# Kernel tuning notes

Hardware: AMD Instinct MI355X
Metric: run time of the kernel (lower is better)

Reference implementation:

```python
import jax, jax.numpy as jnp
import numpy as np

COMMITMENT_COST = 0.25


def setup_inputs() -> dict:
    key = jax.random.key(0)
    k1, k2 = jax.random.split(key)
    z = jax.random.normal(k1, (4096, 512), dtype=jnp.float32)
    # stacked codebooks: [num_codebooks, codebook_size, latent_dim]
    codebooks = jax.random.normal(k2, (8, 16384, 512), dtype=jnp.float32)
    return {"z": z, "codebooks": codebooks}


def reference(z, codebooks):
    """Residual VQ forward. Returns (quantized [B,D], loss scalar, indices [B,K])."""
    z_sg = jax.lax.stop_gradient(z)

    def step(carry, cb):
        residual, quantized, loss = carry
        # squared L2 distances: [B, C]
        d = (jnp.sum(residual * residual, axis=1, keepdims=True)
             + jnp.sum(cb * cb, axis=1)
             - 2.0 * (residual @ cb.T))
        idx = jnp.argmin(d, axis=1)              # [B]
        q_i = cb[idx]                            # gather: [B, D]
        commitment = COMMITMENT_COST * jnp.mean((jax.lax.stop_gradient(q_i) - z) ** 2)
        codebook_l = jnp.mean((q_i - z_sg) ** 2)
        loss = loss + commitment + codebook_l
        return (residual - q_i, quantized + q_i, loss), idx

    init = (z, jnp.zeros_like(z), jnp.float32(0.0))
    (_, quantized, loss), idxs = jax.lax.scan(step, init, codebooks)
    return quantized, loss, idxs.T  # indices: [B, num_codebooks]
```

## Files before the change

kernel.cpp:

```cpp
#include <hip/hip_runtime.h>

typedef _Float16 half8 __attribute__((ext_vector_type(8)));
typedef _Float16 half4v __attribute__((ext_vector_type(4)));
typedef float f32x4 __attribute__((ext_vector_type(4)));

#define MFMA_F16 __builtin_amdgcn_mfma_f32_16x16x32_f16

static constexpr int BATCH  = 4096;
static constexpr int DIM    = 512;
static constexpr int CODES  = 16384;
static constexpr int NCB    = 8;
static constexpr int NCHUNK = 8;
static constexpr int CHUNK  = CODES / NCHUNK;
static constexpr int NT     = CHUNK / 16;
static constexpr int HTILES = NT / 2;
static constexpr int NGROUP = HTILES / 2;
static constexpr int BM     = 128;
static constexpr int NPC    = NCHUNK * 2 * 2;
static constexpr int TILE_H = 8192;
static constexpr int TILE_B = 16384;
static constexpr float LO_SCALE = 2048.0f;
static constexpr float LO_INV   = 1.0f / 2048.0f;
static constexpr float DELTA    = 0.25f;

__device__ __forceinline__ int swz(int code, int kk) {
  return code * DIM + (kk ^ (((code ^ (kk >> 6)) & 7) << 3));
}

__global__ __launch_bounds__(256) void k_init(const float* __restrict__ z,
                                              float* __restrict__ resid,
                                              _Float16* __restrict__ rhi,
                                              _Float16* __restrict__ rlo) {
  int i = blockIdx.x * 256 + threadIdx.x;
  float4 v = ((const float4*)z)[i];
  ((float4*)resid)[i] = v;
  half4v h, l;
  const float* vf = (const float*)&v;
#pragma unroll
  for (int j = 0; j < 4; ++j) {
    float x = vf[j];
    _Float16 hi = (_Float16)x;
    h[j] = hi;
    l[j] = (_Float16)((x - (float)hi) * LO_SCALE);
  }
  *(half4v*)&rhi[(size_t)i * 4] = h;
  *(half4v*)&rlo[(size_t)i * 4] = l;
}

__global__ __launch_bounds__(256) void k_cnorm(const float* __restrict__ cb,
                                               float* __restrict__ cnorm) {
  int wave = threadIdx.x >> 6, lane = threadIdx.x & 63;
  int code = blockIdx.x * 4 + wave;
  const float4* src = (const float4*)(cb + (size_t)code * DIM);
  double s = 0.0;
#pragma unroll
  for (int j = 0; j < 2; ++j) {
    float4 v = src[lane * 2 + j];
    s += (double)v.x * v.x + (double)v.y * v.y + (double)v.z * v.z + (double)v.w * v.w;
  }
#pragma unroll
  for (int off = 32; off; off >>= 1) s += __shfl_down(s, off);
  if (lane == 0) cnorm[code] = (float)s;
}

__global__ __launch_bounds__(256) void k_cvtn(const float* __restrict__ cb,
                                              _Float16* __restrict__ dst,
                                              float* __restrict__ cnorm_k) {
  const int wave  = threadIdx.x >> 6;
  const int lane  = threadIdx.x & 63;
  const int chunk = blockIdx.x & 7;
  const int cidx  = (blockIdx.x >> 3) * 4 + wave;
  const int ntile = cidx >> 4;
  const int code  = cidx & 15;
  const int code_g = chunk * CHUNK + cidx;

  const float* src = cb + (size_t)code_g * DIM + lane * 8;
  float4 v0 = *(const float4*)src;
  float4 v1 = *(const float4*)(src + 4);
  half8 h;
  const float* f0 = (const float*)&v0;
  const float* f1 = (const float*)&v1;
  double s = 0.0;
#pragma unroll
  for (int e = 0; e < 4; ++e) {
    float x = f0[e];
    h[e] = (_Float16)x;
    s += (double)x * x;
    x = f1[e];
    h[e + 4] = (_Float16)x;
    s += (double)x * x;
  }
  const int pos = (lane >> 2) * 512 + (lane & 3) * 128 + code * 8;
  *(half8*)(dst + (size_t)(chunk * NT + ntile) * TILE_H + pos) = h;

#pragma unroll
  for (int off = 32; off; off >>= 1) s += __shfl_down(s, off);
  if (lane == 0) cnorm_k[code_g] = (float)s;
}

#define LEXLT(av, ai, bv, bi) ((av) < (bv) || ((av) == (bv) && (ai) < (bi)))

__global__ __launch_bounds__(256, 2) void k_argmin_pc(
    const _Float16* __restrict__ rhi,
    const _Float16* __restrict__ cvt,
    const float* __restrict__ cnorm,
    float* __restrict__ partmin, int* __restrict__ partidx) {
  __shared__ float Xs[2][4][6][64][4];

  const int tid   = threadIdx.x;
  const int lane  = tid & 63;
  const int kq    = tid >> 6;
  const int chunk = blockIdx.x & 7;
  const int idx   = blockIdx.x >> 3;
  const int mtile = idx >> 1;
  const int half  = idx & 1;
  const int nt0   = half * HTILES;
  const int cbase = chunk * CHUNK;
  const char* ctile = (const char*)(cvt + (size_t)chunk * NT * TILE_H);

  const int kb = (lane >> 4) * 8;
  half8 ah[8][4];
#pragma unroll
  for (int band = 0; band < 8; ++band) {
    const size_t rbase =
        (size_t)(mtile * BM + band * 16 + (lane & 15)) * DIM + kq * 128;
#pragma unroll
    for (int t = 0; t < 4; ++t)
      ah[band][t] = *(const half8*)(rhi + rbase + t * 32 + kb);
  }

  const int qbase = kq * 4096 + lane * 16;
  const int rcode = lane & 15;

  float tv0[2][4], tv1[2][4];
  int   ti0[2][4], ti1[2][4];
#pragma unroll
  for (int j = 0; j < 2; ++j)
#pragma unroll
    for (int r = 0; r < 4; ++r) {
      tv0[j][r] = tv1[j][r] = 3.4e38f;
      ti0[j][r] = ti1[j][r] = 0x7fffffff;
    }

  half8 s0h[2], s1h[2];

#define LOAD_HT(SH, NTI, H)                                                  \
  {                                                                          \
    const char* bp_ = ctile + (size_t)(NTI) * TILE_B + qbase + (H) * 2048;   \
    SH[0] = *(const half8*)(bp_);                                            \
    SH[1] = *(const half8*)(bp_ + 1024);                                     \
  }

#define MFMA_HT(SH, TB)                                                      \
  {                                                                          \
    __builtin_amdgcn_s_setprio(1);                                           \
    _Pragma("unroll")                                                        \
    for (int j_ = 0; j_ < 2; ++j_) {                                         \
      _Pragma("unroll")                                                      \
      for (int b_ = 0; b_ < 8; ++b_)                                         \
        acch[b_] = MFMA_F16(ah[b_][(TB) + j_], SH[j_], acch[b_], 0, 0, 0);   \
    }                                                                        \
    __builtin_amdgcn_s_setprio(0);                                           \
  }

#define TOP2_INS(d, cg, J, R)                                                \
  {                                                                          \
    bool b0_ = (d) < tv0[J][R];                                              \
    bool b1_ = (d) < tv1[J][R];                                              \
    tv1[J][R] = b0_ ? tv0[J][R] : (b1_ ? (d) : tv1[J][R]);                   \
    ti1[J][R] = b0_ ? ti0[J][R] : (b1_ ? (cg) : ti1[J][R]);                  \
    tv0[J][R] = b0_ ? (d) : tv0[J][R];                                       \
    ti0[J][R] = b0_ ? (cg) : ti0[J][R];                                      \
  }

  LOAD_HT(s0h, nt0, 0);
  float cn_a = cnorm[cbase + nt0 * 16 + rcode];
  float cn_b = cnorm[cbase + (nt0 + 1) * 16 + rcode];

  for (int g = 0; g < NGROUP; ++g) {
    const int ta = nt0 + 2 * g;
    const int tb = ta + 1;
    const bool more = (g + 1 < NGROUP);
    float cn_na = more ? cnorm[cbase + (ta + 2) * 16 + rcode] : 0.f;
    float cn_nb = more ? cnorm[cbase + (ta + 3) * 16 + rcode] : 0.f;

    f32x4 acch[8];
    f32x4 dha0, dha1, dhb0, dhb1;

#pragma unroll
    for (int b = 0; b < 8; ++b) acch[b] = (f32x4){0.f, 0.f, 0.f, 0.f};
    LOAD_HT(s1h, ta, 1);
    MFMA_HT(s0h, 0);
    LOAD_HT(s0h, tb, 0);
    MFMA_HT(s1h, 2);
#pragma unroll
    for (int b = 0; b < 8; ++b) {
      if ((b >> 1) == kq) {
        if ((b & 1) == 0) dha0 = acch[b]; else dha1 = acch[b];
      } else {
        const int slot = b - (((b >> 1) > kq) ? 2 : 0);
        *(f32x4*)&Xs[0][kq][slot][lane][0] = acch[b];
      }
    }

#pragma unroll
    for (int b = 0; b < 8; ++b) acch[b] = (f32x4){0.f, 0.f, 0.f, 0.f};
    LOAD_HT(s1h, tb, 1);
    MFMA_HT(s0h, 0);
    const int pn = more ? ta + 2 : tb;
    LOAD_HT(s0h, pn, 0);
    MFMA_HT(s1h, 2);
#pragma unroll
    for (int b = 0; b < 8; ++b) {
      if ((b >> 1) == kq) {
        if ((b & 1) == 0) dhb0 = acch[b]; else dhb1 = acch[b];
      } else {
        const int slot = b - (((b >> 1) > kq) ? 2 : 0);
        *(f32x4*)&Xs[1][kq][slot][lane][0] = acch[b];
      }
    }

    asm volatile("s_waitcnt lgkmcnt(0)" ::: "memory");
    __builtin_amdgcn_s_barrier();
    __builtin_amdgcn_sched_barrier(0);

    f32x4 dta[2] = {dha0, dha1};
    f32x4 dtb[2] = {dhb0, dhb1};
#pragma unroll
    for (int j = 0; j < 2; ++j) {
      const int ob = 2 * kq + j;
      for (int kq2 = 0; kq2 < 4; ++kq2) {
        if (kq2 == kq) continue;
        const int slot = ob - ((kq > kq2) ? 2 : 0);
        dta[j] += *(const f32x4*)&Xs[0][kq2][slot][lane][0];
        dtb[j] += *(const f32x4*)&Xs[1][kq2][slot][lane][0];
      }
    }
    __builtin_amdgcn_sched_barrier(0);
    __builtin_amdgcn_s_barrier();
    __builtin_amdgcn_sched_barrier(0);

    const int cga = cbase + ta * 16 + rcode;
    const int cgb = cga + 16;
#pragma unroll
    for (int j = 0; j < 2; ++j) {
#pragma unroll
      for (int r = 0; r < 4; ++r) {
        float d = cn_a - 2.0f * dta[j][r];
        TOP2_INS(d, cga, j, r);
      }
#pragma unroll
      for (int r = 0; r < 4; ++r) {
        float d = cn_b - 2.0f * dtb[j][r];
        TOP2_INS(d, cgb, j, r);
      }
    }
    cn_a = cn_na;
    cn_b = cn_nb;
  }
#undef LOAD_HT
#undef MFMA_HT
#undef TOP2_INS

#pragma unroll
  for (int s = 1; s < 16; s <<= 1) {
#pragma unroll
    for (int j = 0; j < 2; ++j) {
#pragma unroll
      for (int r = 0; r < 4; ++r) {
        float b0v = __shfl_xor(tv0[j][r], s), b1v = __shfl_xor(tv1[j][r], s);
        int   b0i = __shfl_xor(ti0[j][r], s), b1i = __shfl_xor(ti1[j][r], s);
        bool p0 = LEXLT(tv0[j][r], ti0[j][r], b0v, b0i);
        float r0v = p0 ? tv0[j][r] : b0v;  int r0i = p0 ? ti0[j][r] : b0i;
        float xv  = p0 ? b0v : tv0[j][r];  int xi  = p0 ? b0i : ti0[j][r];
        bool p1 = LEXLT(tv1[j][r], ti1[j][r], b1v, b1i);
        float yv = p1 ? tv1[j][r] : b1v;   int yi = p1 ? ti1[j][r] : b1i;
        bool p2 = LEXLT(xv, xi, yv, yi);
        float r1v = p2 ? xv : yv;          int r1i = p2 ? xi : yi;
        tv0[j][r] = r0v; ti0[j][r] = r0i;
        tv1[j][r] = r1v; ti1[j][r] = r1i;
      }
    }
  }
  if ((lane & 15) == 0) {
    const int pslot = chunk * 2 + half;
#pragma unroll
    for (int j = 0; j < 2; ++j) {
      const int rowbase = mtile * BM + (2 * kq + j) * 16 + (lane >> 4) * 4;
#pragma unroll
      for (int r = 0; r < 4; ++r) {
        const size_t base = (size_t)(rowbase + r) * NPC + pslot * 2;
        partmin[base + 0] = tv0[j][r]; partidx[base + 0] = ti0[j][r];
        partmin[base + 1] = tv1[j][r]; partidx[base + 1] = ti1[j][r];
      }
    }
  }
}

__device__ __forceinline__ void load8(const float* __restrict__ cb, int cbase, int nt,
                                      int s_code, int s_kseg, float4 v[8]) {
  const float4* src = (const float4*)(cb + (size_t)(cbase + nt * 16 + s_code) * DIM + s_kseg);
#pragma unroll
  for (int j = 0; j < 8; ++j) v[j] = src[j];
}

__device__ __forceinline__ void cvt_store(_Float16* __restrict__ BHbuf,
                                          _Float16* __restrict__ BLbuf,
                                          int code, int kseg, const float4 sv[8]) {
  const float* f = (const float*)sv;
#pragma unroll
  for (int j = 0; j < 4; ++j) {
    half8 h, l;
#pragma unroll
    for (int e = 0; e < 8; ++e) {
      float x = f[j * 8 + e];
      _Float16 hi = (_Float16)x;
      h[e] = hi;
      l[e] = (_Float16)((x - (float)hi) * LO_SCALE);
    }
    int hw = swz(code, kseg + j * 8);
    *(half8*)(BHbuf + hw) = h;
    *(half8*)(BLbuf + hw) = l;
  }
}

__global__ __launch_bounds__(256, 2) void k_argmin_fb(
    const _Float16* __restrict__ rhi, const _Float16* __restrict__ rlo,
    const float* __restrict__ cb, const float* __restrict__ cnorm,
    float* __restrict__ partmin, int* __restrict__ partidx) {
  __shared__ _Float16 BH[2][16 * DIM];
  __shared__ _Float16 BL[2][16 * DIM];
  __shared__ float CN[CHUNK];

  const int tid   = threadIdx.x;
  const int lane  = tid & 63;
  const int wave  = tid >> 6;
  const int mtile = blockIdx.x >> 3;
  const int chunk = blockIdx.x & 7;
  const int cbase = chunk * CHUNK;

  {
    const float4* s = (const float4*)(cnorm + cbase);
    float4* d = (float4*)CN;
    for (int i = tid; i < CHUNK / 4; i += 256) d[i] = s[i];
  }

  const int arow = mtile * 64 + wave * 16 + (lane & 15);
  const int kb = (lane >> 4) * 8;
  half8 ah[16], al[16];
#pragma unroll
  for (int t = 0; t < 16; ++t) {
    ah[t] = *(const half8*)(rhi + (size_t)arow * DIM + t * 32 + kb);
    al[t] = *(const half8*)(rlo + (size_t)arow * DIM + t * 32 + kb);
  }

  const int s_code = tid >> 4;
  const int s_kseg = (tid & 15) * 32;

  float rmin[4] = {3.4e38f, 3.4e38f, 3.4e38f, 3.4e38f};
  int   ridx[4] = {0, 0, 0, 0};

  {
    float4 v0[8];
    load8(cb, cbase, 0, s_code, s_kseg, v0);
    cvt_store(&BH[0][0], &BL[0][0], s_code, s_kseg, v0);
  }

  const int rcode = lane & 15;
  for (int nt = 0; nt < NT; ++nt) {
    __syncthreads();
    const int cur = nt & 1;
    const bool more = (nt + 1 < NT);
    float4 nv[8];
    if (more) load8(cb, cbase, nt + 1, s_code, s_kseg, nv);

    f32x4 acch  = {0.f, 0.f, 0.f, 0.f};
    f32x4 accl0 = {0.f, 0.f, 0.f, 0.f};
    f32x4 accl1 = {0.f, 0.f, 0.f, 0.f};
    const _Float16* bh = &BH[cur][0];
    const _Float16* bl = &BL[cur][0];
#pragma unroll
    for (int t = 0; t < 16; ++t) {
      const int hw = swz(rcode, t * 32 + kb);
      half8 fbh = *(const half8*)(bh + hw);
      half8 fbl = *(const half8*)(bl + hw);
      acch  = MFMA_F16(ah[t], fbh, acch, 0, 0, 0);
      accl0 = MFMA_F16(ah[t], fbl, accl0, 0, 0, 0);
      accl1 = MFMA_F16(al[t], fbh, accl1, 0, 0, 0);
    }
    float cn = CN[nt * 16 + rcode];
    int codeg = cbase + nt * 16 + rcode;
#pragma unroll
    for (int r = 0; r < 4; ++r) {
      float d = cn - 2.0f * (acch[r] + (accl0[r] + accl1[r]) * LO_INV);
      if (d < rmin[r]) { rmin[r] = d; ridx[r] = codeg; }
    }
    if (more) cvt_store(&BH[cur ^ 1][0], &BL[cur ^ 1][0], s_code, s_kseg, nv);
  }

#pragma unroll
  for (int s = 1; s < 16; s <<= 1) {
#pragma unroll
    for (int r = 0; r < 4; ++r) {
      float ov = __shfl_xor(rmin[r], s);
      int   oi = __shfl_xor(ridx[r], s);
      if (ov < rmin[r] || (ov == rmin[r] && oi < ridx[r])) { rmin[r] = ov; ridx[r] = oi; }
    }
  }
  if ((lane & 15) == 0) {
    int rowbase = mtile * 64 + wave * 16 + (lane >> 4) * 4;
#pragma unroll
    for (int r = 0; r < 4; ++r) {
#pragma unroll
      for (int t = 0; t < 4; ++t) {
        partmin[(size_t)(rowbase + r) * NPC + chunk * 4 + t] = rmin[r];
        partidx[(size_t)(rowbase + r) * NPC + chunk * 4 + t] = ridx[r];
      }
    }
  }
}

__global__ __launch_bounds__(256) void k_update(
    const float* __restrict__ cb, const float* __restrict__ z,
    const float* __restrict__ partmin, const int* __restrict__ partidx,
    float* __restrict__ resid, _Float16* __restrict__ rhi, _Float16* __restrict__ rlo,
    float* __restrict__ quant, float* __restrict__ out_idx,
    float* __restrict__ losspart, int step) {
  __shared__ int   s_idx[16];
  __shared__ int   s_cand[16][32];
  __shared__ int   s_cnt[16];
  __shared__ float s_red[4];
  const int tid = threadIdx.x;
  const int row0 = blockIdx.x * 16;

  if (tid < 16) {
    const int row = row0 + tid;
    float m = 3.4e38f;
    for (int c = 0; c < NPC; ++c) {
      float v = partmin[(size_t)row * NPC + c];
      if (v < m) m = v;
    }
    int cnt = 0;
    for (int c = 0; c < NPC; ++c) {
      float v = partmin[(size_t)row * NPC + c];
      if (v < m + DELTA) s_cand[tid][cnt++] = partidx[(size_t)row * NPC + c];
    }
    s_cnt[tid] = cnt;
  }
  __syncthreads();

  {
    const int wv = tid >> 6, ln = tid & 63;
    for (int rr = wv; rr < 16; rr += 4) {
      const int row = row0 + rr;
      const float* rrow = resid + (size_t)row * DIM + ln * 8;
      double bestd = 1.0e300;
      int    besti = 0x7fffffff;
      const int cnt = s_cnt[rr];
      for (int c = 0; c < cnt; ++c) {
        const int ci = s_cand[rr][c];
        const float* crow = cb + (size_t)ci * DIM + ln * 8;
        double s = 0.0;
#pragma unroll
        for (int e = 0; e < 8; ++e) {
          double df = (double)rrow[e] - (double)crow[e];
          s += df * df;
        }
#pragma unroll
        for (int off = 32; off; off >>= 1) s += __shfl_down(s, off);
        s = __shfl(s, 0);
        if (s < bestd || (s == bestd && ci < besti)) { bestd = s; besti = ci; }
      }
      if (ln == 0) {
        s_idx[rr] = besti;
        out_idx[(size_t)row * NCB + step] = (float)besti;
      }
    }
  }
  __syncthreads();

  float lsum = 0.f;
  const int sub = tid >> 7;
  const int e   = tid & 127;
  for (int rp = 0; rp < 16; rp += 2) {
    const int rl = rp + sub;
    const int row = row0 + rl;
    const int idx = s_idx[rl];
    float4 q  = ((const float4*)cb)[(size_t)idx * 128 + e];
    float4 zv = ((const float4*)z)[(size_t)row * 128 + e];
    float4 rv = ((const float4*)resid)[(size_t)row * 128 + e];
    float4 nr, qa;
    const float* qf = (const float*)&q;
    const float* zf = (const float*)&zv;
    const float* rf = (const float*)&rv;
    float* nf = (float*)&nr;
    float* af = (float*)&qa;
    if (step == 0) {
#pragma unroll
      for (int j = 0; j < 4; ++j) af[j] = qf[j];
    } else {
      float4 old = ((const float4*)quant)[(size_t)row * 128 + e];
      const float* of = (const float*)&old;
#pragma unroll
      for (int j = 0; j < 4; ++j) af[j] = of[j] + qf[j];
    }
    ((float4*)quant)[(size_t)row * 128 + e] = qa;
    half4v h, l;
#pragma unroll
    for (int j = 0; j < 4; ++j) {
      float nrj = rf[j] - qf[j];
      nf[j] = nrj;
      _Float16 hi = (_Float16)nrj;
      h[j] = hi;
      l[j] = (_Float16)((nrj - (float)hi) * LO_SCALE);
      float dq = qf[j] - zf[j];
      lsum += dq * dq;
    }
    ((float4*)resid)[(size_t)row * 128 + e] = nr;
    *(half4v*)&rhi[(size_t)row * DIM + e * 4] = h;
    *(half4v*)&rlo[(size_t)row * DIM + e * 4] = l;
  }
#pragma unroll
  for (int off = 32; off; off >>= 1) lsum += __shfl_down(lsum, off);
  if ((tid & 63) == 0) s_red[tid >> 6] = lsum;
  __syncthreads();
  if (tid == 0) losspart[blockIdx.x] = s_red[0] + s_red[1] + s_red[2] + s_red[3];
}

__global__ __launch_bounds__(256) void k_loss(const float* __restrict__ losspart,
                                              float* __restrict__ out_loss) {
  __shared__ double red[4];
  const int tid = threadIdx.x;
  double s = 0.0;
  for (int i = tid; i < NCB * 256; i += 256) s += (double)losspart[i];
#pragma unroll
  for (int off = 32; off; off >>= 1) s += __shfl_down(s, off);
  if ((tid & 63) == 0) red[tid >> 6] = s;
  __syncthreads();
  if (tid == 0)
    out_loss[0] = (float)((red[0] + red[1] + red[2] + red[3]) *
                          (1.25 / (double)((size_t)BATCH * DIM)));
}

extern "C" void kernel_launch(void* const* d_in, const int* in_sizes, int n_in,
                              void* d_out, int out_size, void* d_ws, size_t ws_size,
                              hipStream_t stream) {
  const float* z  = (const float*)d_in[0];
  const float* cb = (const float*)d_in[1];
  float* out = (float*)d_out;
  float* quant    = out;
  float* out_loss = out + (size_t)BATCH * DIM;
  float* out_idx  = out + (size_t)BATCH * DIM + 1;

  char* ws = (char*)d_ws;
  float*    resid    = (float*)ws;
  _Float16* rhi      = (_Float16*)(ws + ((size_t)8  << 20));
  _Float16* rlo      = (_Float16*)(ws + ((size_t)12 << 20));
  float*    cnorm    = (float*)(ws + ((size_t)16 << 20));
  float*    partmin  = (float*)(ws + ((size_t)17 << 20));
  int*      partidx  = (int*)  (ws + ((size_t)18 << 20));
  float*    losspart = (float*)(ws + ((size_t)19 << 20));
  _Float16* cvtbuf   = (_Float16*)(ws + ((size_t)20 << 20));

  const size_t REQ = ((size_t)20 << 20) + ((size_t)16 << 20);
  const bool pre = (ws_size >= REQ);

  k_init<<<dim3((BATCH * DIM / 4) / 256), dim3(256), 0, stream>>>(z, resid, rhi, rlo);
  if (!pre)
    k_cnorm<<<dim3(NCB * CODES / 4), dim3(256), 0, stream>>>(cb, cnorm);

  for (int k = 0; k < NCB; ++k) {
    const float* cbk = cb + (size_t)k * CODES * DIM;
    if (pre) {
      k_cvtn<<<dim3(CODES * 64 / 256), dim3(256), 0, stream>>>(
          cbk, cvtbuf, cnorm + (size_t)k * CODES);
      k_argmin_pc<<<dim3((BATCH / BM) * NCHUNK * 2), dim3(256), 0, stream>>>(
          rhi, cvtbuf, cnorm + (size_t)k * CODES, partmin, partidx);
    } else {
      k_argmin_fb<<<dim3((BATCH / 64) * NCHUNK), dim3(256), 0, stream>>>(
          rhi, rlo, cbk, cnorm + (size_t)k * CODES, partmin, partidx);
    }
    k_update<<<dim3(BATCH / 16), dim3(256), 0, stream>>>(
        cbk, z, partmin, partidx, resid, rhi, rlo,
        quant, out_idx, losspart + k * 256, k);
  }
  k_loss<<<dim3(1), dim3(256), 0, stream>>>(losspart, out_loss);
}
```

Before: 993.2 us.

## Split argmin waves into 2 row-groups by 2 K-halves to cut LDS reduction

The argmin kernel's work split across the four waves changes from four K-quarters covering all 8 row bands to two K-halves times two row-groups of 4 bands each. Each wave now computes 4 band accumulators over 256 of K instead of 8 over 128. The cross-wave partial-sum exchange through shared memory falls from 6 stores and 6 loads per tile pair to 2 of each with one partner wave. In exchange each wave loads twice as many codebook fragments per tile, and the total MFMA count stays the same.

Result: slower. 2.566 ms (+158.3%).

```diff
diff --git a/kernel.cpp b/kernel.cpp
--- a/kernel.cpp
+++ b/kernel.cpp
@@ -105,11 +105,14 @@
     const _Float16* __restrict__ cvt,
     const float* __restrict__ cnorm,
     float* __restrict__ partmin, int* __restrict__ partidx) {
-  __shared__ float Xs[2][4][6][64][4];
+  __shared__ float Xs[2][4][2][64][4];
 
   const int tid   = threadIdx.x;
   const int lane  = tid & 63;
-  const int kq    = tid >> 6;
+  const int wave  = tid >> 6;
+  const int wp    = wave >> 1;
+  const int kh    = wave & 1;
+  const int partner = wp * 2 + (kh ^ 1);
   const int chunk = blockIdx.x & 7;
   const int idx   = blockIdx.x >> 3;
   const int mtile = idx >> 1;
@@ -119,18 +122,20 @@
   const char* ctile = (const char*)(cvt + (size_t)chunk * NT * TILE_H);
 
   const int kb = (lane >> 4) * 8;
-  half8 ah[8][4];
-#pragma unroll
-  for (int band = 0; band < 8; ++band) {
+  half8 ah[4][8];
+#pragma unroll
+  for (int lb = 0; lb < 4; ++lb) {
     const size_t rbase =
-        (size_t)(mtile * BM + band * 16 + (lane & 15)) * DIM + kq * 128;
-#pragma unroll
-    for (int t = 0; t < 4; ++t)
-      ah[band][t] = *(const half8*)(rhi + rbase + t * 32 + kb);
-  }
-
-  const int qbase = kq * 4096 + lane * 16;
+        (size_t)(mtile * BM + (4 * wp + lb) * 16 + (lane & 15)) * DIM + kh * 256;
+#pragma unroll
+    for (int t = 0; t < 8; ++t)
+      ah[lb][t] = *(const half8*)(rhi + rbase + t * 32 + kb);
+  }
+
+  const int qbase = kh * 8192 + lane * 16;
   const int rcode = lane & 15;
+
+  const int ownbase = kh * 2;
 
   float tv0[2][4], tv1[2][4];
   int   ti0[2][4], ti1[2][4];
@@ -142,22 +147,24 @@
       ti0[j][r] = ti1[j][r] = 0x7fffffff;
     }
 
-  half8 s0h[2], s1h[2];
+  half8 s0h[4], s1h[4];
 
 #define LOAD_HT(SH, NTI, H)                                                  \
   {                                                                          \
-    const char* bp_ = ctile + (size_t)(NTI) * TILE_B + qbase + (H) * 2048;   \
+    const char* bp_ = ctile + (size_t)(NTI) * TILE_B + qbase + (H) * 4096;   \
     SH[0] = *(const half8*)(bp_);                                            \
     SH[1] = *(const half8*)(bp_ + 1024);                                     \
+    SH[2] = *(const half8*)(bp_ + 2048);                                     \
+    SH[3] = *(const half8*)(bp_ + 3072);                                     \
   }
 
 #define MFMA_HT(SH, TB)                                                      \
   {                                                                          \
     __builtin_amdgcn_s_setprio(1);                                           \
     _Pragma("unroll")                                                        \
-    for (int j_ = 0; j_ < 2; ++j_) {                                         \
+    for (int j_ = 0; j_ < 4; ++j_) {                                         \
       _Pragma("unroll")                                                      \
-      for (int b_ = 0; b_ < 8; ++b_)                                         \
+      for (int b_ = 0; b_ < 4; ++b_)                                         \
         acch[b_] = MFMA_F16(ah[b_][(TB) + j_], SH[j_], acch[b_], 0, 0, 0);   \
     }                                                                        \
     __builtin_amdgcn_s_setprio(0);                                           \
@@ -184,58 +191,48 @@
     float cn_na = more ? cnorm[cbase + (ta + 2) * 16 + rcode] : 0.f;
     float cn_nb = more ? cnorm[cbase + (ta + 3) * 16 + rcode] : 0.f;
 
-    f32x4 acch[8];
-    f32x4 dha0, dha1, dhb0, dhb1;
-
-#pragma unroll
-    for (int b = 0; b < 8; ++b) acch[b] = (f32x4){0.f, 0.f, 0.f, 0.f};
+    f32x4 acch[4];
+    f32x4 owna0, owna1, ownb0, ownb1;
+
+#pragma unroll
+    for (int b = 0; b < 4; ++b) acch[b] = (f32x4){0.f, 0.f, 0.f, 0.f};
     LOAD_HT(s1h, ta, 1);
     MFMA_HT(s0h, 0);
     LOAD_HT(s0h, tb, 0);
-    MFMA_HT(s1h, 2);
-#pragma unroll
-    for (int b = 0; b < 8; ++b) {
-      if ((b >> 1) == kq) {
-        if ((b & 1) == 0) dha0 = acch[b]; else dha1 = acch[b];
-      } else {
-        const int slot = b - (((b >> 1) > kq) ? 2 : 0);
-        *(f32x4*)&Xs[0][kq][slot][lane][0] = acch[b];
-      }
-    }
-
-#pragma unroll
-    for (int b = 0; b < 8; ++b) acch[b] = (f32x4){0.f, 0.f, 0.f, 0.f};
+    MFMA_HT(s1h, 4);
+    owna0 = acch[ownbase];
+    owna1 = acch[ownbase + 1];
+    {
+      const int fb = 2 - ownbase;
+      *(f32x4*)&Xs[0][wave][0][lane][0] = acch[fb];
+      *(f32x4*)&Xs[0][wave][1][lane][0] = acch[fb + 1];
+    }
+
+#pragma unroll
+    for (int b = 0; b < 4; ++b) acch[b] = (f32x4){0.f, 0.f, 0.f, 0.f};
     LOAD_HT(s1h, tb, 1);
     MFMA_HT(s0h, 0);
     const int pn = more ? ta + 2 : tb;
     LOAD_HT(s0h, pn, 0);
-    MFMA_HT(s1h, 2);
-#pragma unroll
-    for (int b = 0; b < 8; ++b) {
-      if ((b >> 1) == kq) {
-        if ((b & 1) == 0) dhb0 = acch[b]; else dhb1 = acch[b];
-      } else {
-        const int slot = b - (((b >> 1) > kq) ? 2 : 0);
-        *(f32x4*)&Xs[1][kq][slot][lane][0] = acch[b];
-      }
+    MFMA_HT(s1h, 4);
+    ownb0 = acch[ownbase];
+    ownb1 = acch[ownbase + 1];
+    {
+      const int fb = 2 - ownbase;
+      *(f32x4*)&Xs[1][wave][0][lane][0] = acch[fb];
+      *(f32x4*)&Xs[1][wave][1][lane][0] = acch[fb + 1];
     }
 
     asm volatile("s_waitcnt lgkmcnt(0)" ::: "memory");
     __builtin_amdgcn_s_barrier();
     __builtin_amdgcn_sched_barrier(0);
 
-    f32x4 dta[2] = {dha0, dha1};
-    f32x4 dtb[2] = {dhb0, dhb1};
-#pragma unroll
-    for (int j = 0; j < 2; ++j) {
-      const int ob = 2 * kq + j;
-      for (int kq2 = 0; kq2 < 4; ++kq2) {
-        if (kq2 == kq) continue;
-        const int slot = ob - ((kq > kq2) ? 2 : 0);
-        dta[j] += *(const f32x4*)&Xs[0][kq2][slot][lane][0];
-        dtb[j] += *(const f32x4*)&Xs[1][kq2][slot][lane][0];
-      }
-    }
+    f32x4 dta[2], dtb[2];
+    dta[0] = owna0 + *(const f32x4*)&Xs[0][partner][0][lane][0];
+    dta[1] = owna1 + *(const f32x4*)&Xs[0][partner][1][lane][0];
+    dtb[0] = ownb0 + *(const f32x4*)&Xs[1][partner][0][lane][0];
+    dtb[1] = ownb1 + *(const f32x4*)&Xs[1][partner][1][lane][0];
+
     __builtin_amdgcn_sched_barrier(0);
     __builtin_amdgcn_s_barrier();
     __builtin_amdgcn_sched_barrier(0);
@@ -286,7 +283,8 @@
     const int pslot = chunk * 2 + half;
 #pragma unroll
     for (int j = 0; j < 2; ++j) {
-      const int rowbase = mtile * BM + (2 * kq + j) * 16 + (lane >> 4) * 4;
+      const int gband = 4 * wp + ownbase + j;
+      const int rowbase = mtile * BM + gband * 16 + (lane >> 4) * 4;
 #pragma unroll
       for (int r = 0; r < 4; ++r) {
         const size_t base = (size_t)(rowbase + r) * NPC + pslot * 2;
```

## Convert all codebooks upfront and split argmin into quarter-chunk blocks

Applied to the files above, without the earlier changes.

Moves the fp16 conversion of all eight codebooks into a single launch before the loop, writing into a larger workspace image. This removes seven per-step conversion launches and the serial dependency between conversion and argmin. Each argmin chunk is also split into quarters instead of halves, doubling the grid for more parallelism, at the cost of twice as many partial candidates that the update kernel must scan. It needs a much larger workspace, about 148 MB, and otherwise falls back to the slower path.

Measured after the change: 1.184 ms. 1.19x slower.

```diff
diff --git a/kernel.cpp b/kernel.cpp
--- a/kernel.cpp
+++ b/kernel.cpp
@@ -13,12 +13,13 @@
 static constexpr int NCHUNK = 8;
 static constexpr int CHUNK  = CODES / NCHUNK;
 static constexpr int NT     = CHUNK / 16;
-static constexpr int HTILES = NT / 2;
-static constexpr int NGROUP = HTILES / 2;
+static constexpr int QTILES = NT / 4;
+static constexpr int NGROUP = QTILES / 2;
 static constexpr int BM     = 128;
-static constexpr int NPC    = NCHUNK * 2 * 2;
+static constexpr int NPC    = NCHUNK * 4 * 2;
 static constexpr int TILE_H = 8192;
 static constexpr int TILE_B = 16384;
+static constexpr size_t CBIMG_H = (size_t)NCHUNK * NT * TILE_H;
 static constexpr float LO_SCALE = 2048.0f;
 static constexpr float LO_INV   = 1.0f / 2048.0f;
 static constexpr float DELTA    = 0.25f;
@@ -65,16 +66,18 @@
 
 __global__ __launch_bounds__(256) void k_cvtn(const float* __restrict__ cb,
                                               _Float16* __restrict__ dst,
-                                              float* __restrict__ cnorm_k) {
+                                              float* __restrict__ cnorm_all) {
   const int wave  = threadIdx.x >> 6;
   const int lane  = threadIdx.x & 63;
   const int chunk = blockIdx.x & 7;
-  const int cidx  = (blockIdx.x >> 3) * 4 + wave;
+  const int b2    = blockIdx.x >> 3;
+  const int kcb   = b2 >> 9;
+  const int cidx  = (b2 & 511) * 4 + wave;
   const int ntile = cidx >> 4;
   const int code  = cidx & 15;
   const int code_g = chunk * CHUNK + cidx;
 
-  const float* src = cb + (size_t)code_g * DIM + lane * 8;
+  const float* src = cb + (size_t)kcb * CODES * DIM + (size_t)code_g * DIM + lane * 8;
   float4 v0 = *(const float4*)src;
   float4 v1 = *(const float4*)(src + 4);
   half8 h;
@@ -91,11 +94,12 @@
     s += (double)x * x;
   }
   const int pos = (lane >> 2) * 512 + (lane & 3) * 128 + code * 8;
-  *(half8*)(dst + (size_t)(chunk * NT + ntile) * TILE_H + pos) = h;
+  *(half8*)(dst + (size_t)kcb * CBIMG_H +
+            (size_t)(chunk * NT + ntile) * TILE_H + pos) = h;
 
 #pragma unroll
   for (int off = 32; off; off >>= 1) s += __shfl_down(s, off);
-  if (lane == 0) cnorm_k[code_g] = (float)s;
+  if (lane == 0) cnorm_all[(size_t)kcb * CODES + code_g] = (float)s;
 }
 
 #define LEXLT(av, ai, bv, bi) ((av) < (bv) || ((av) == (bv) && (ai) < (bi)))
@@ -112,9 +116,9 @@
   const int kq    = tid >> 6;
   const int chunk = blockIdx.x & 7;
   const int idx   = blockIdx.x >> 3;
-  const int mtile = idx >> 1;
-  const int half  = idx & 1;
-  const int nt0   = half * HTILES;
+  const int mtile = idx >> 2;
+  const int quart = idx & 3;
+  const int nt0   = quart * QTILES;
   const int cbase = chunk * CHUNK;
   const char* ctile = (const char*)(cvt + (size_t)chunk * NT * TILE_H);
 
@@ -283,7 +287,7 @@
     }
   }
   if ((lane & 15) == 0) {
-    const int pslot = chunk * 2 + half;
+    const int pslot = chunk * 4 + quart;
 #pragma unroll
     for (int j = 0; j < 2; ++j) {
       const int rowbase = mtile * BM + (2 * kq + j) * 16 + (lane >> 4) * 4;
@@ -412,9 +416,9 @@
 #pragma unroll
     for (int r = 0; r < 4; ++r) {
 #pragma unroll
-      for (int t = 0; t < 4; ++t) {
-        partmin[(size_t)(rowbase + r) * NPC + chunk * 4 + t] = rmin[r];
-        partidx[(size_t)(rowbase + r) * NPC + chunk * 4 + t] = ridx[r];
+      for (int t = 0; t < 8; ++t) {
+        partmin[(size_t)(rowbase + r) * NPC + chunk * 8 + t] = rmin[r];
+        partidx[(size_t)(rowbase + r) * NPC + chunk * 8 + t] = ridx[r];
       }
     }
   }
@@ -427,7 +431,7 @@
     float* __restrict__ quant, float* __restrict__ out_idx,
     float* __restrict__ losspart, int step) {
   __shared__ int   s_idx[16];
-  __shared__ int   s_cand[16][32];
+  __shared__ int   s_cand[16][64];
   __shared__ int   s_cnt[16];
   __shared__ float s_red[4];
   const int tid = threadIdx.x;
@@ -562,20 +566,22 @@
   float*    losspart = (float*)(ws + ((size_t)19 << 20));
   _Float16* cvtbuf   = (_Float16*)(ws + ((size_t)20 << 20));
 
-  const size_t REQ = ((size_t)20 << 20) + ((size_t)16 << 20);
+  const size_t REQ = ((size_t)20 << 20) + ((size_t)NCB * 16 << 20);
   const bool pre = (ws_size >= REQ);
 
   k_init<<<dim3((BATCH * DIM / 4) / 256), dim3(256), 0, stream>>>(z, resid, rhi, rlo);
-  if (!pre)
+  if (pre) {
+    k_cvtn<<<dim3(NCB * CODES * 64 / 256), dim3(256), 0, stream>>>(cb, cvtbuf, cnorm);
+  } else {
     k_cnorm<<<dim3(NCB * CODES / 4), dim3(256), 0, stream>>>(cb, cnorm);
+  }
 
   for (int k = 0; k < NCB; ++k) {
     const float* cbk = cb + (size_t)k * CODES * DIM;
     if (pre) {
-      k_cvtn<<<dim3(CODES * 64 / 256), dim3(256), 0, stream>>>(
-          cbk, cvtbuf, cnorm + (size_t)k * CODES);
-      k_argmin_pc<<<dim3((BATCH / BM) * NCHUNK * 2), dim3(256), 0, stream>>>(
-          rhi, cvtbuf, cnorm + (size_t)k * CODES, partmin, partidx);
+      k_argmin_pc<<<dim3((BATCH / BM) * NCHUNK * 4), dim3(256), 0, stream>>>(
+          rhi, cvtbuf + (size_t)k * CBIMG_H, cnorm + (size_t)k * CODES,
+          partmin, partidx);
     } else {
       k_argmin_fb<<<dim3((BATCH / 64) * NCHUNK), dim3(256), 0, stream>>>(
           rhi, rlo, cbk, cnorm + (size_t)k * CODES, partmin, partidx);
```
